# Optimization experiments

Measured on AMD Instinct MI355X. Metric: run time of the kernel, lower is better.

## Reference

```python
import jax, jax.numpy as jnp
import numpy as np

MEAN_LOG = 0.0
STD_LOG = 1.0
D = 32          # context_size (SRU hidden)
K = 64          # num_mix_components
H = 3 * K       # MLP hidden width
LOG_2PI = float(np.log(2.0 * np.pi))


def clamp_preserve_gradients(x, lo, hi):
    # forward clamp, straight-through gradient
    return x + jax.lax.stop_gradient(jnp.clip(x, lo, hi) - x)


def setup_inputs() -> dict:
    key = jax.random.key(0)
    ks = jax.random.split(key, 10)
    B, S = 128, 4096
    inter_times = jax.random.uniform(ks[0], (B, S), dtype=jnp.float32)
    mask = jnp.ones((B, S), dtype=jnp.float32)
    ages_u = jax.random.uniform(ks[1], (B, S), dtype=jnp.float32)
    # SRU parameters (input_size=1, hidden=D, k=4 since 1 != D)
    W = jax.random.normal(ks[2], (1, 4 * D), dtype=jnp.float32) / np.sqrt(1.0)
    v = 0.1 * jax.random.normal(ks[3], (2 * D,), dtype=jnp.float32)   # weight_c (v_f, v_r)
    b = jnp.zeros((2 * D,), dtype=jnp.float32)                         # bias (b_f, b_r)
    context_init = jnp.zeros((D,), dtype=jnp.float32)
    # MLP: (D+1) -> H -> H -> H
    W1 = jax.random.normal(ks[4], (D + 1, H), dtype=jnp.float32) / np.sqrt(D + 1)
    b1 = jnp.zeros((H,), dtype=jnp.float32)
    W2 = jax.random.normal(ks[5], (H, H), dtype=jnp.float32) / np.sqrt(H)
    b2 = jnp.zeros((H,), dtype=jnp.float32)
    W3 = jax.random.normal(ks[6], (H, H), dtype=jnp.float32) / np.sqrt(H)
    b3 = jnp.zeros((H,), dtype=jnp.float32)
    return dict(inter_times=inter_times, mask=mask, ages_u=ages_u, W=W, v=v, b=b,
                context_init=context_init, W1=W1, b1=b1, W2=W2, b2=b2, W3=W3, b3=b3)


def reference(inter_times, mask, ages_u, W, v, b, context_init, W1, b1, W2, b2, W3, b3):
    B, S = inter_times.shape
    # --- features: normalized log inter-event times ---
    feats = (jnp.log(inter_times + 1e-8) - MEAN_LOG) / STD_LOG        # (B,S)
    x = feats[..., None]                                              # (B,S,1)
    # --- SRU: one big input projection, then elementwise recurrence via scan ---
    U = (x @ W).reshape(B, S, 4, D)                                   # (B,S,4,D)
    U = jnp.transpose(U, (1, 0, 2, 3))                                # (S,B,4,D) time-major
    vf, vr = v[:D], v[D:]
    bf, br = b[:D], b[D:]

    def step(c, u):
        u0, u1, u2, u3 = u[:, 0], u[:, 1], u[:, 2], u[:, 3]
        f = jax.nn.sigmoid(u1 + vf * c + bf)
        c_new = f * c + (1.0 - f) * u0
        r = jax.nn.sigmoid(u2 + vr * c_new + br)
        h = r * c_new + (1.0 - r) * u3                                # highway (identity activation)
        return c_new, h

    c0 = jnp.zeros((B, D), dtype=feats.dtype)
    _, hs = jax.lax.scan(step, c0, U)                                 # (S,B,D)
    context = jnp.transpose(hs, (1, 0, 2))                            # (B,S,D)
    # remove_last: shift right, prepend learned init context
    context = jnp.concatenate(
        [jnp.broadcast_to(context_init, (B, 1, D)), context[:, :-1, :]], axis=1)
    # --- age features / residual times ---
    ages = inter_times - inter_times * ages_u                         # elapsed age
    residual_times = inter_times - ages                               # = inter_times * ages_u
    ages_f = (jnp.log(ages + 1e-8) - MEAN_LOG) / STD_LOG
    ctx = jnp.concatenate([context, ages_f[..., None]], axis=-1)      # (B,S,D+1)
    # --- mixture-parameter MLP ---
    h1 = jax.nn.relu(ctx @ W1 + b1)
    h2 = jax.nn.relu(h1 @ W2 + b2)
    raw = h2 @ W3 + b3                                                # (B,S,3K)
    locs = raw[..., :K]
    log_scales = clamp_preserve_gradients(raw[..., K:2 * K], -5.0, 3.0)
    log_w = jax.nn.log_softmax(raw[..., 2 * K:], axis=-1)
    # --- log-normal mixture log-prob ---
    t = jnp.clip(residual_times, 1e-10, None)
    y = jnp.log(t)
    z = (y - MEAN_LOG) / STD_LOG
    zs = (z[..., None] - locs) * jnp.exp(-log_scales)
    comp = log_w - log_scales - 0.5 * LOG_2PI - 0.5 * zs * zs         # (B,S,K)
    log_p = jax.scipy.special.logsumexp(comp, axis=-1) - jnp.log(STD_LOG) - y
    log_p = log_p * mask
    return log_p.sum(-1)                                              # (B,)
```

## Files before the change

### kernel.cpp

```cpp
#include <hip/hip_runtime.h>
#include <hip/hip_bf16.h>
#include <math.h>
#include <type_traits>

#define Bn 128
#define Sn 4096
#define Dn 32
#define Hn 192
#define ASTR 196
#define CH 32
#define CHL 128
#define BURN 128
#define HALF_LOG2PI 0.9189385332046727f

typedef __attribute__((ext_vector_type(8))) short short8v;
typedef __attribute__((ext_vector_type(4))) float f32x4;

__device__ __forceinline__ unsigned short f2bf(float x) {
    return (unsigned short)((__float_as_uint(x) + 0x8000u) >> 16);
}
__device__ __forceinline__ unsigned pack_bf2(float lo, float hi) {
    __hip_bfloat162 h = __float22bfloat162_rn(float2{lo, hi});
    return *reinterpret_cast<unsigned*>(&h);
}

__global__ __launch_bounds__(64) void pack_weights(
    const float* __restrict__ W1, const float* __restrict__ W2,
    const float* __restrict__ W3, unsigned short* __restrict__ wp)
{
    int fid = blockIdx.x, lane = threadIdx.x;
    const float* Wsrc; int Krows, f;
    if (fid < 24)      { Wsrc = W1; Krows = 33;  f = fid; }
    else if (fid < 96) { Wsrc = W2; Krows = 192; f = fid - 24; }
    else               { Wsrc = W3; Krows = 192; f = fid - 96; }
    int kstep = f / 12, nb = f % 12;
    int k0 = kstep * 32 + 8 * (lane >> 4);
    int n  = nb * 16 + (lane & 15);
    short8v v;
#pragma unroll
    for (int j = 0; j < 8; ++j) {
        int k = k0 + j;
        float x = (k < Krows) ? Wsrc[k * Hn + n] : 0.0f;
        v[j] = (short)f2bf(x);
    }
    *(short8v*)(wp + (size_t)fid * 512 + lane * 8) = v;
}

__global__ __launch_bounds__(256) void recurrence_kernel(
    const float* __restrict__ it_g, const float* __restrict__ W,
    const float* __restrict__ v,    const float* __restrict__ bia,
    const float* __restrict__ cinit, unsigned short* __restrict__ ctx)
{
    const float LOG2E = 1.4426950408889634f;
    int g = blockIdx.x * 256 + threadIdx.x;
    int d = g & 31;
    int bc = g >> 5;
    int b = bc & (Bn - 1);
    int chunk = bc >> 7;

    float w0 = W[d], w3 = W[96 + d];
    float nw1l = -W[32 + d] * LOG2E, nw2l = -W[64 + d] * LOG2E;
    float nvfl = -v[d] * LOG2E,      nvrl = -v[32 + d] * LOG2E;
    float nbfl = -bia[d] * LOG2E,    nbrl = -bia[32 + d] * LOG2E;

    const f32x4* itv = (const f32x4*)(it_g + (size_t)b * Sn);
    unsigned short* cp = ctx + ((size_t)b * Sn) * Dn + d;
    int s_start = chunk * CHL;
    int s_end   = s_start + CHL;
    int sbeg    = (chunk == 0) ? 0 : s_start - BURN;
    if (chunk == 0) cp[0] = f2bf(cinit[d]);

    float c = 0.0f;
    int blk0 = sbeg >> 3, blkN = s_end >> 3;
    f32x4 A0 = itv[blk0 * 2], A1 = itv[blk0 * 2 + 1];
    for (int blk = blk0; blk < blkN; ++blk) {
        f32x4 N0 = A0, N1 = A1;
        if (blk + 1 < blkN) { N0 = itv[blk * 2 + 2]; N1 = itv[blk * 2 + 3]; }
        float feat[8];
#pragma unroll
        for (int j = 0; j < 4; ++j) {
            feat[j]     = __logf(A0[j] + 1e-8f);
            feat[j + 4] = __logf(A1[j] + 1e-8f);
        }
        unsigned short hb[8];
#pragma unroll
        for (int j = 0; j < 8; ++j) {
            float ft = feat[j];
            float u0 = ft * w0, u3 = ft * w3;
            float nxfl = fmaf(ft, nw1l, nbfl);
            float nxrl = fmaf(ft, nw2l, nbrl);
            float sfn = fmaf(nvfl, c, nxfl);
            float ef  = __builtin_amdgcn_exp2f(sfn);
            float f_  = __builtin_amdgcn_rcpf(1.0f + ef);
            float cmu = c - u0;
            float cn  = fmaf(f_, cmu, u0);
            float srn = fmaf(nvrl, cn, nxrl);
            float er  = __builtin_amdgcn_exp2f(srn);
            float r_  = __builtin_amdgcn_rcpf(1.0f + er);
            float h   = fmaf(r_, cn - u3, u3);
            c = cn;
            hb[j] = f2bf(h);
        }
        int s0 = blk * 8;
        if (s0 >= s_start) {
#pragma unroll
            for (int j = 0; j < 8; ++j)
                if (s0 + j + 1 < Sn) cp[(size_t)(s0 + j + 1) * Dn] = hb[j];
        }
        A0 = N0; A1 = N1;
    }
}

__global__ __launch_bounds__(128, 2) void mlp_kernel(
    const float* __restrict__ it_g, const float* __restrict__ mask_g,
    const float* __restrict__ au_g, const unsigned short* __restrict__ ctxb,
    const unsigned short* __restrict__ wp,
    const float* __restrict__ b1, const float* __restrict__ b2,
    const float* __restrict__ b3, float* __restrict__ out)
{
    __shared__ __align__(16) unsigned short Acts[64 * ASTR];
    __shared__ float wsum[2];

    const int tid = threadIdx.x;
    const int lane = tid & 63;
    const int wv = tid >> 6;
    const int gq = lane >> 4;
    const int cl = lane & 15;
    const long tile = (long)blockIdx.x * 64;
    const int b = (int)(tile >> 12);

#define NBM(j) ((j) + (((j) >= 2) ? 2 : 0) + (((j) >= 4) ? 2 : 0) + 2 * wv)

    {
        int tok = tid >> 1, h = tid & 1;
        unsigned short* row = Acts + tok * ASTR;
        const unsigned short* src = ctxb + (tile + tok) * Dn + h * 16;
        *(short8v*)(row + h * 16)     = *(const short8v*)src;
        *(short8v*)(row + h * 16 + 8) = *(const short8v*)(src + 8);
        short8v z = {0, 0, 0, 0, 0, 0, 0, 0};
        if (h == 0) {
            float itv = it_g[tile + tok];
            float auv = au_g[tile + tok];
            short8v za = z;
            za[0] = (short)f2bf(__logf(fmaf(-auv, itv, itv) + 1e-8f));
            *(short8v*)(row + 32) = za;
        } else {
            *(short8v*)(row + 40) = z;
            *(short8v*)(row + 48) = z;
            *(short8v*)(row + 56) = z;
        }
    }
    __syncthreads();

    f32x4 acc[6][4];

    auto run_layer = [&](auto NKC, const unsigned short* wpl,
                         const float* __restrict__ bias) {
        constexpr int nk = NKC.value;
#pragma unroll
        for (int j = 0; j < 6; ++j) {
            f32x4 bb = *(const f32x4*)(bias + NBM(j) * 16 + 4 * gq);
#pragma unroll
            for (int m = 0; m < 4; ++m) acc[j][m] = bb;
        }
#pragma unroll
        for (int ks = 0; ks < nk; ++ks) {
            short8v bfv[4];
#pragma unroll
            for (int m = 0; m < 4; ++m)
                bfv[m] = *(const short8v*)(Acts + (m * 16 + cl) * ASTR + ks * 32 + 8 * gq);
            const unsigned short* wk = wpl + (size_t)ks * (12 * 512) + lane * 8;
#pragma unroll
            for (int j = 0; j < 6; ++j) {
                short8v af = *(const short8v*)(wk + NBM(j) * 512);
#pragma unroll
                for (int m = 0; m < 4; ++m)
                    acc[j][m] = __builtin_amdgcn_mfma_f32_16x16x32_bf16(af, bfv[m], acc[j][m], 0, 0, 0);
            }
        }
    };

    auto store_h = [&]() {
#pragma unroll
        for (int j = 0; j < 6; ++j) {
            int fbase = NBM(j) * 16 + 4 * gq;
#pragma unroll
            for (int m = 0; m < 4; ++m) {
                f32x4 vv = acc[j][m];
#pragma unroll
                for (int r = 0; r < 4; ++r) vv[r] = fmaxf(vv[r], 0.0f);
                uint2 pk;
                pk.x = pack_bf2(vv[0], vv[1]);
                pk.y = pack_bf2(vv[2], vv[3]);
                *(uint2*)(Acts + (m * 16 + cl) * ASTR + fbase) = pk;
            }
        }
    };

    run_layer(std::integral_constant<int, 2>{}, wp, b1);
    __syncthreads();
    store_h();
    __syncthreads();
    run_layer(std::integral_constant<int, 6>{}, wp + 24 * 512, b2);
    __syncthreads();
    store_h();
    __syncthreads();
    run_layer(std::integral_constant<int, 6>{}, wp + 96 * 512, b3);

    float lseA[4], lseB[4];
#pragma unroll
    for (int m = 0; m < 4; ++m) {
        long tok = tile + m * 16 + cl;
        float itv = it_g[tok];
        float auv = au_g[tok];
        float y = __logf(fmaxf(itv * auv, 1e-10f));

        float m1 = -1e30f;
#pragma unroll
        for (int j = 4; j < 6; ++j)
#pragma unroll
            for (int r = 0; r < 4; ++r) m1 = fmaxf(m1, acc[j][m][r]);
        m1 = fmaxf(m1, __shfl_xor(m1, 16, 64));
        m1 = fmaxf(m1, __shfl_xor(m1, 32, 64));

        float sa = 0.0f, sb = 0.0f;
#pragma unroll
        for (int j = 0; j < 2; ++j) {
#pragma unroll
            for (int r = 0; r < 4; ++r) {
                float loc = acc[j][m][r];
                float lsr = fminf(fmaxf(acc[2 + j][m][r], -5.0f), 3.0f);
                float lg  = acc[4 + j][m][r];
                float zs = (y - loc) * __expf(-lsr);
                float g = -lsr - HALF_LOG2PI - 0.5f * zs * zs;
                sa += __expf(lg - m1);
                sb += __expf(lg - m1 + g);
            }
        }
        sa += __shfl_xor(sa, 16, 64); sa += __shfl_xor(sa, 32, 64);
        sb += __shfl_xor(sb, 16, 64); sb += __shfl_xor(sb, 32, 64);
        lseA[m] = m1 + __logf(sa);
        lseB[m] = m1 + __logf(sb);
    }

    float* X = (float*)Acts;
    __syncthreads();
    if (gq == 0) {
#pragma unroll
        for (int m = 0; m < 4; ++m) {
            float2 pr; pr.x = lseA[m]; pr.y = lseB[m];
            *(float2*)(X + (m * 16 + cl) * 4 + wv * 2) = pr;
        }
    }
    __syncthreads();

    {
        int t = wv * 32 + (lane & 31);
        long tok = tile + t;
        f32x4 pr = *(const f32x4*)(X + t * 4);
        float ma = fmaxf(pr[0], pr[2]);
        float lse_a = ma + __logf(__expf(pr[0] - ma) + __expf(pr[2] - ma));
        float mb = fmaxf(pr[1], pr[3]);
        float lse_b = mb + __logf(__expf(pr[1] - mb) + __expf(pr[3] - mb));

        float itv = it_g[tok];
        float auv = au_g[tok];
        float mk  = mask_g[tok];
        float y = __logf(fmaxf(itv * auv, 1e-10f));

        float lp = (lse_b - lse_a - y) * mk;
        float psum = (lane < 32) ? lp : 0.0f;
#pragma unroll
        for (int mm = 1; mm < 64; mm <<= 1) psum += __shfl_xor(psum, mm, 64);
        if (lane == 0) wsum[wv] = psum;
    }
    __syncthreads();
    if (tid == 0) atomicAdd(out + b, wsum[0] + wsum[1]);
#undef NBM
}

extern "C" void kernel_launch(void* const* d_in, const int* in_sizes, int n_in,
                              void* d_out, int out_size, void* d_ws, size_t ws_size,
                              hipStream_t stream) {
    const float* it_g  = (const float*)d_in[0];
    const float* mask  = (const float*)d_in[1];
    const float* au    = (const float*)d_in[2];
    const float* W     = (const float*)d_in[3];
    const float* v     = (const float*)d_in[4];
    const float* bia   = (const float*)d_in[5];
    const float* cinit = (const float*)d_in[6];
    const float* W1    = (const float*)d_in[7];
    const float* b1    = (const float*)d_in[8];
    const float* W2    = (const float*)d_in[9];
    const float* b2    = (const float*)d_in[10];
    const float* W3    = (const float*)d_in[11];
    const float* b3    = (const float*)d_in[12];
    float* out = (float*)d_out;

    unsigned short* ctxb = (unsigned short*)d_ws;
    unsigned short* wp   = ctxb + (size_t)Bn * Sn * Dn;

    hipMemsetAsync(d_out, 0, (size_t)out_size * sizeof(float), stream);

    pack_weights<<<168, 64, 0, stream>>>(W1, W2, W3, wp);
    recurrence_kernel<<<(Bn * Dn * CH) / 256, 256, 0, stream>>>(
        it_g, W, v, bia, cinit, ctxb);
    mlp_kernel<<<(Bn * Sn) / 64, 128, 0, stream>>>(
        it_g, mask, au, ctxb, wp, b1, b2, b3, out);
}
```

Before: 186.0 us.

## Retile MLP kernel to 128-token blocks with four waves and interleaved N mapping

Doubles the tokens per block to 128 and uses four waves, each computing three output column blocks across eight token tiles. This increases reuse of each loaded weight fragment and halves the number of blocks and atomics. Column blocks are interleaved so each wave holds matching loc, scale and logit slices. Input scalars are prefetched before the last layer to hide latency, at the cost of higher register pressure and a larger LDS footprint.

```diff
diff --git a/kernel.cpp b/kernel.cpp
--- a/kernel.cpp
+++ b/kernel.cpp
@@ -111,25 +111,25 @@
     }
 }
 
-__global__ __launch_bounds__(128, 2) void mlp_kernel(
+__global__ __launch_bounds__(256, 2) void mlp_kernel(
     const float* __restrict__ it_g, const float* __restrict__ mask_g,
     const float* __restrict__ au_g, const unsigned short* __restrict__ ctxb,
     const unsigned short* __restrict__ wp,
     const float* __restrict__ b1, const float* __restrict__ b2,
     const float* __restrict__ b3, float* __restrict__ out)
 {
-    __shared__ __align__(16) unsigned short Acts[64 * ASTR];
-    __shared__ float wsum[2];
+    __shared__ __align__(16) unsigned short Acts[128 * ASTR];
+    __shared__ float wsum[4];
 
     const int tid = threadIdx.x;
     const int lane = tid & 63;
     const int wv = tid >> 6;
     const int gq = lane >> 4;
     const int cl = lane & 15;
-    const long tile = (long)blockIdx.x * 64;
+    const long tile = (long)blockIdx.x * 128;
     const int b = (int)(tile >> 12);
 
-#define NBM(j) ((j) + (((j) >= 2) ? 2 : 0) + (((j) >= 4) ? 2 : 0) + 2 * wv)
+#define NBM(j) (wv + 4 * (j))
 
     {
         int tok = tid >> 1, h = tid & 1;
@@ -152,29 +152,29 @@
     }
     __syncthreads();
 
-    f32x4 acc[6][4];
+    f32x4 acc[3][8];
 
     auto run_layer = [&](auto NKC, const unsigned short* wpl,
                          const float* __restrict__ bias) {
         constexpr int nk = NKC.value;
 #pragma unroll
-        for (int j = 0; j < 6; ++j) {
+        for (int j = 0; j < 3; ++j) {
             f32x4 bb = *(const f32x4*)(bias + NBM(j) * 16 + 4 * gq);
 #pragma unroll
-            for (int m = 0; m < 4; ++m) acc[j][m] = bb;
+            for (int m = 0; m < 8; ++m) acc[j][m] = bb;
         }
 #pragma unroll
         for (int ks = 0; ks < nk; ++ks) {
-            short8v bfv[4];
-#pragma unroll
-            for (int m = 0; m < 4; ++m)
+            short8v bfv[8];
+#pragma unroll
+            for (int m = 0; m < 8; ++m)
                 bfv[m] = *(const short8v*)(Acts + (m * 16 + cl) * ASTR + ks * 32 + 8 * gq);
             const unsigned short* wk = wpl + (size_t)ks * (12 * 512) + lane * 8;
 #pragma unroll
-            for (int j = 0; j < 6; ++j) {
+            for (int j = 0; j < 3; ++j) {
                 short8v af = *(const short8v*)(wk + NBM(j) * 512);
 #pragma unroll
-                for (int m = 0; m < 4; ++m)
+                for (int m = 0; m < 8; ++m)
                     acc[j][m] = __builtin_amdgcn_mfma_f32_16x16x32_bf16(af, bfv[m], acc[j][m], 0, 0, 0);
             }
         }
@@ -182,10 +182,10 @@
 
     auto store_h = [&]() {
 #pragma unroll
-        for (int j = 0; j < 6; ++j) {
+        for (int j = 0; j < 3; ++j) {
             int fbase = NBM(j) * 16 + 4 * gq;
 #pragma unroll
-            for (int m = 0; m < 4; ++m) {
+            for (int m = 0; m < 8; ++m) {
                 f32x4 vv = acc[j][m];
 #pragma unroll
                 for (int r = 0; r < 4; ++r) vv[r] = fmaxf(vv[r], 0.0f);
@@ -205,37 +205,43 @@
     __syncthreads();
     store_h();
     __syncthreads();
+
+    float itp[8], aup[8];
+#pragma unroll
+    for (int m = 0; m < 8; ++m) {
+        itp[m] = it_g[tile + m * 16 + cl];
+        aup[m] = au_g[tile + m * 16 + cl];
+    }
+    float it2 = 0.0f, au2 = 0.0f, mk2 = 0.0f;
+    if (tid < 128) {
+        it2 = it_g[tile + tid];
+        au2 = au_g[tile + tid];
+        mk2 = mask_g[tile + tid];
+    }
+
     run_layer(std::integral_constant<int, 6>{}, wp + 96 * 512, b3);
 
-    float lseA[4], lseB[4];
-#pragma unroll
-    for (int m = 0; m < 4; ++m) {
-        long tok = tile + m * 16 + cl;
-        float itv = it_g[tok];
-        float auv = au_g[tok];
-        float y = __logf(fmaxf(itv * auv, 1e-10f));
+    float lseA[8], lseB[8];
+#pragma unroll
+    for (int m = 0; m < 8; ++m) {
+        float y = __logf(fmaxf(itp[m] * aup[m], 1e-10f));
 
         float m1 = -1e30f;
 #pragma unroll
-        for (int j = 4; j < 6; ++j)
-#pragma unroll
-            for (int r = 0; r < 4; ++r) m1 = fmaxf(m1, acc[j][m][r]);
+        for (int r = 0; r < 4; ++r) m1 = fmaxf(m1, acc[2][m][r]);
         m1 = fmaxf(m1, __shfl_xor(m1, 16, 64));
         m1 = fmaxf(m1, __shfl_xor(m1, 32, 64));
 
         float sa = 0.0f, sb = 0.0f;
 #pragma unroll
-        for (int j = 0; j < 2; ++j) {
-#pragma unroll
-            for (int r = 0; r < 4; ++r) {
-                float loc = acc[j][m][r];
-                float lsr = fminf(fmaxf(acc[2 + j][m][r], -5.0f), 3.0f);
-                float lg  = acc[4 + j][m][r];
-                float zs = (y - loc) * __expf(-lsr);
-                float g = -lsr - HALF_LOG2PI - 0.5f * zs * zs;
-                sa += __expf(lg - m1);
-                sb += __expf(lg - m1 + g);
-            }
+        for (int r = 0; r < 4; ++r) {
+            float loc = acc[0][m][r];
+            float lsr = fminf(fmaxf(acc[1][m][r], -5.0f), 3.0f);
+            float lg  = acc[2][m][r];
+            float zs = (y - loc) * __expf(-lsr);
+            float g = -lsr - HALF_LOG2PI - 0.5f * zs * zs;
+            sa += __expf(lg - m1);
+            sb += __expf(lg - m1 + g);
         }
         sa += __shfl_xor(sa, 16, 64); sa += __shfl_xor(sa, 32, 64);
         sb += __shfl_xor(sb, 16, 64); sb += __shfl_xor(sb, 32, 64);
@@ -247,35 +253,36 @@
     __syncthreads();
     if (gq == 0) {
 #pragma unroll
-        for (int m = 0; m < 4; ++m) {
+        for (int m = 0; m < 8; ++m) {
             float2 pr; pr.x = lseA[m]; pr.y = lseB[m];
-            *(float2*)(X + (m * 16 + cl) * 4 + wv * 2) = pr;
+            *(float2*)(X + (m * 16 + cl) * 8 + wv * 2) = pr;
         }
     }
     __syncthreads();
 
     {
-        int t = wv * 32 + (lane & 31);
-        long tok = tile + t;
-        f32x4 pr = *(const f32x4*)(X + t * 4);
-        float ma = fmaxf(pr[0], pr[2]);
-        float lse_a = ma + __logf(__expf(pr[0] - ma) + __expf(pr[2] - ma));
-        float mb = fmaxf(pr[1], pr[3]);
-        float lse_b = mb + __logf(__expf(pr[1] - mb) + __expf(pr[3] - mb));
-
-        float itv = it_g[tok];
-        float auv = au_g[tok];
-        float mk  = mask_g[tok];
-        float y = __logf(fmaxf(itv * auv, 1e-10f));
-
-        float lp = (lse_b - lse_a - y) * mk;
-        float psum = (lane < 32) ? lp : 0.0f;
+        float lp = 0.0f;
+        if (tid < 128) {
+            f32x4 p0 = *(const f32x4*)(X + tid * 8);
+            f32x4 p1 = *(const f32x4*)(X + tid * 8 + 4);
+            float ma = fmaxf(fmaxf(p0[0], p0[2]), fmaxf(p1[0], p1[2]));
+            float sa = __expf(p0[0] - ma) + __expf(p0[2] - ma) +
+                       __expf(p1[0] - ma) + __expf(p1[2] - ma);
+            float mb = fmaxf(fmaxf(p0[1], p0[3]), fmaxf(p1[1], p1[3]));
+            float sb = __expf(p0[1] - mb) + __expf(p0[3] - mb) +
+                       __expf(p1[1] - mb) + __expf(p1[3] - mb);
+            float lse_a = ma + __logf(sa);
+            float lse_b = mb + __logf(sb);
+            float y = __logf(fmaxf(it2 * au2, 1e-10f));
+            lp = (lse_b - lse_a - y) * mk2;
+        }
+        float psum = lp;
 #pragma unroll
         for (int mm = 1; mm < 64; mm <<= 1) psum += __shfl_xor(psum, mm, 64);
         if (lane == 0) wsum[wv] = psum;
     }
     __syncthreads();
-    if (tid == 0) atomicAdd(out + b, wsum[0] + wsum[1]);
+    if (tid == 0) atomicAdd(out + b, wsum[0] + wsum[1] + wsum[2] + wsum[3]);
 #undef NBM
 }
 
@@ -305,6 +312,6 @@
     pack_weights<<<168, 64, 0, stream>>>(W1, W2, W3, wp);
     recurrence_kernel<<<(Bn * Dn * CH) / 256, 256, 0, stream>>>(
         it_g, W, v, bia, cinit, ctxb);
-    mlp_kernel<<<(Bn * Sn) / 64, 128, 0, stream>>>(
+    mlp_kernel<<<(Bn * Sn) / 128, 256, 0, stream>>>(
         it_g, mask, au, ctxb, wp, b1, b2, b3, out);
 }
```

Result: no change. 184.6 us (-0.8%).
